# Performance work log

Measured on AMD Instinct MI355X. Metric: run time of the kernel, lower is better.

Reference implementation:

```python
import jax, jax.numpy as jnp
import numpy as np

N, C, H, W = 512, 64, 32, 32
HID, HEADS = 128, 4
E = 16384
BN_EPS = 1e-5


def conv2d(x, w, b, pad):
    y = jax.lax.conv_general_dilated(x, w, (1, 1), [(pad, pad), (pad, pad)],
                                     dimension_numbers=('NCHW', 'OIHW', 'NCHW'))
    return y + b[None, :, None, None]


def bn_eval(x, g, b):
    # inference BN with running_mean=0, running_var=1
    scale = g * (1.0 / np.sqrt(1.0 + BN_EPS))
    return x * scale[None, :, None, None] + b[None, :, None, None]


def gat_layer(x, src, dst, lin_w, att_s, att_d, bias):
    # x: (N, in) -> (N, HID); PyG GATConv heads=4, concat=False, add_self_loops
    h = (x @ lin_w).reshape(N, HEADS, HID)          # (N, H, D)
    a_s = jnp.einsum('nhd,hd->nh', h, att_s)        # source score
    a_d = jnp.einsum('nhd,hd->nh', h, att_d)        # target score
    e = jax.nn.leaky_relu(a_s[src] + a_d[dst], 0.2)  # (E', H)
    m = jax.ops.segment_max(e, dst, num_segments=N)
    ex = jnp.exp(e - m[dst])
    denom = jax.ops.segment_sum(ex, dst, num_segments=N)
    alpha = ex / (denom[dst] + 1e-16)               # per-target softmax
    out = jax.ops.segment_sum(alpha[:, :, None] * h[src], dst, num_segments=N)
    return out.mean(axis=1) + bias                  # concat=False -> head mean


def setup_inputs() -> dict:
    key = jax.random.key(0)
    ks = jax.random.split(key, 24)
    s = lambda *shape: 0.05
    d = {}
    d['x'] = jax.random.normal(ks[0], (N, C, H, W), jnp.float32)
    d['edge_index'] = jax.random.randint(ks[1], (2, E), 0, N, jnp.int64)
    d['confidence_maps'] = jax.random.uniform(ks[2], (N, 1, H, W), jnp.float32)
    # feature encoder: 1x1 conv + BN
    d['fe_w'] = jax.random.normal(ks[3], (HID, C, 1, 1), jnp.float32) * 0.05
    d['fe_b'] = jnp.zeros((HID,), jnp.float32)
    d['fe_g'] = jnp.ones((HID,), jnp.float32)
    d['fe_beta'] = jnp.zeros((HID,), jnp.float32)
    # spatial processor: two 3x3 conv + BN
    d['sp_w1'] = jax.random.normal(ks[4], (HID, HID, 3, 3), jnp.float32) * 0.02
    d['sp_b1'] = jnp.zeros((HID,), jnp.float32)
    d['sp_g1'] = jnp.ones((HID,), jnp.float32)
    d['sp_be1'] = jnp.zeros((HID,), jnp.float32)
    d['sp_w2'] = jax.random.normal(ks[5], (HID, HID, 3, 3), jnp.float32) * 0.02
    d['sp_b2'] = jnp.zeros((HID,), jnp.float32)
    d['sp_g2'] = jnp.ones((HID,), jnp.float32)
    d['sp_be2'] = jnp.zeros((HID,), jnp.float32)
    # GAT layers (in=HID, out=HID, heads=HEADS)
    d['g1_lin'] = jax.random.normal(ks[6], (HID, HEADS * HID), jnp.float32) * 0.05
    d['g1_as'] = jax.random.normal(ks[7], (HEADS, HID), jnp.float32) * 0.05
    d['g1_ad'] = jax.random.normal(ks[8], (HEADS, HID), jnp.float32) * 0.05
    d['g1_b'] = jnp.zeros((HID,), jnp.float32)
    d['g2_lin'] = jax.random.normal(ks[9], (HID, HEADS * HID), jnp.float32) * 0.05
    d['g2_as'] = jax.random.normal(ks[10], (HEADS, HID), jnp.float32) * 0.05
    d['g2_ad'] = jax.random.normal(ks[11], (HEADS, HID), jnp.float32) * 0.05
    d['g2_b'] = jnp.zeros((HID,), jnp.float32)
    # output projector 1x1 conv
    d['op_w'] = jax.random.normal(ks[12], (C, HID, 1, 1), jnp.float32) * 0.05
    d['op_b'] = jnp.zeros((C,), jnp.float32)
    return d


def reference(x, edge_index, confidence_maps, fe_w, fe_b, fe_g, fe_beta,
              sp_w1, sp_b1, sp_g1, sp_be1, sp_w2, sp_b2, sp_g2, sp_be2,
              g1_lin, g1_as, g1_ad, g1_b, g2_lin, g2_as, g2_ad, g2_b,
              op_w, op_b):
    # feature encoder + confidence modulation
    xe = jax.nn.relu(bn_eval(conv2d(x, fe_w, fe_b, 0), fe_g, fe_beta))
    xe = xe * confidence_maps
    # spatial processor
    xp = jax.nn.relu(bn_eval(conv2d(xe, sp_w1, sp_b1, 1), sp_g1, sp_be1))
    xp = jax.nn.relu(bn_eval(conv2d(xp, sp_w2, sp_b2, 1), sp_g2, sp_be2))
    # global avg pool -> node features (N, HID)
    x_node = xp.mean(axis=(2, 3))
    # add self loops once
    sl = jnp.arange(N, dtype=edge_index.dtype)
    src = jnp.concatenate([edge_index[0], sl])
    dst = jnp.concatenate([edge_index[1], sl])
    xg = jax.nn.relu(gat_layer(x_node, src, dst, g1_lin, g1_as, g1_ad, g1_b))
    xg = jax.nn.relu(gat_layer(xg, src, dst, g2_lin, g2_as, g2_ad, g2_b))
    # broadcast-add GNN output back onto spatial maps
    x_comb = xg[:, :, None, None] + xp
    return conv2d(x_comb, op_w, op_b, 0)
```

## Files before the change

### kernel.cpp

```cpp
#include <hip/hip_runtime.h>
#include <stdint.h>

#define NIMG 512
#define CINCH 64
#define HIDC 128
#define NEDGE 16384
#define HWPIX 1024
#define PW2 34
#define PPIX 1156
#define APITCH 272
#define AROW 9248

typedef __attribute__((ext_vector_type(8))) short bf16x8;
typedef __attribute__((ext_vector_type(4))) float f32x4;
typedef __attribute__((ext_vector_type(16))) float f32x16;

static __device__ __forceinline__ unsigned short f2bf(float f){
  unsigned u = __builtin_bit_cast(unsigned, f);
  u += 0x7FFFu + ((u>>16)&1u);
  return (unsigned short)(u>>16);
}
static __device__ __forceinline__ float bf2f(unsigned short s){
  unsigned u = ((unsigned)s)<<16;
  return __builtin_bit_cast(float, u);
}

static __device__ __forceinline__ void gload16(const char* src, char* dst){
  __builtin_amdgcn_global_load_lds(
      (const __attribute__((address_space(1))) unsigned int*)src,
      (__attribute__((address_space(3))) unsigned int*)dst, 16, 0, 0);
}

__global__ void k_init(unsigned short* xe_pad, unsigned short* xp1_pad,
                       float* xnode_acc, int* cnt, int* pos){
  int idx = blockIdx.x*256 + threadIdx.x;
  int total_b = NIMG*132*16;
  for(int i = idx; i < total_b; i += gridDim.x*256){
    int img = i / (132*16);
    int rem = i - img*(132*16);
    int bp = rem >> 4;
    int slot = rem & 15;
    int r, c;
    if(bp < 34){ r = 0; c = bp; }
    else if(bp < 68){ r = 33; c = bp-34; }
    else if(bp < 100){ r = bp-68+1; c = 0; }
    else { r = bp-100+1; c = 33; }
    size_t off = ((size_t)img*PPIX + r*PW2 + c)*128 + slot*8;
    uint4 z = {0,0,0,0};
    *(uint4*)(xe_pad + off) = z;
    *(uint4*)(xp1_pad + off) = z;
  }
  for(int i = idx; i < NIMG*HIDC; i += gridDim.x*256) xnode_acc[i] = 0.f;
  for(int i = idx; i < NIMG; i += gridDim.x*256){ cnt[i] = 0; pos[i] = 0; }
}

__global__ void k_wconv(const float* __restrict__ sp_w1, const float* __restrict__ sp_w2,
                        const float* __restrict__ fe_w, const float* __restrict__ op_w,
                        unsigned short* Wb1, unsigned short* Wb2,
                        unsigned short* Wfe, unsigned short* Wop){
  int idx = blockIdx.x*256 + threadIdx.x;
  for(int i = idx; i < 147456; i += gridDim.x*256){
    int j = i & 7, slot = (i>>3)&15, co = (i>>7)&127, tap = i>>14;
    int cin = (((slot - 3*co) & 15)<<3) + j;
    Wb1[i] = f2bf(sp_w1[(co*128+cin)*9 + tap]);
    Wb2[i] = f2bf(sp_w2[(co*128+cin)*9 + tap]);
  }
  for(int i = idx; i < 8192; i += gridDim.x*256){
    int j = i & 7, s = (i>>3)&7, co = i>>6;
    int ci = ((s ^ (co&7))<<3) + j;
    Wfe[i] = f2bf(fe_w[co*64+ci]);
  }
  for(int i = idx; i < 8192; i += gridDim.x*256){
    int j = i & 7, s = (i>>3)&15, co = i>>7;
    int cin = ((s ^ (co&7))<<3) + j;
    Wop[i] = f2bf(op_w[co*128+cin]);
  }
}

__global__ void k_csr_count(const int* __restrict__ ei, int* cnt){
  int e = blockIdx.x*256 + threadIdx.x;
  if(e < NEDGE) atomicAdd(&cnt[ei[NEDGE+e]], 1);
}
__global__ void k_csr_scan(const int* __restrict__ cnt, int* offs){
  __shared__ int sc[512];
  int t = threadIdx.x;
  sc[t] = cnt[t] + 1;
  __syncthreads();
  for(int o = 1; o < 512; o <<= 1){
    int add = (t >= o) ? sc[t-o] : 0;
    __syncthreads();
    sc[t] += add;
    __syncthreads();
  }
  if(t == 0) offs[0] = 0;
  offs[t+1] = sc[t];
}
__global__ void k_csr_fill(const int* __restrict__ ei, const int* __restrict__ offs,
                           int* pos, int* csr_src){
  int e = blockIdx.x*256 + threadIdx.x;
  if(e < NEDGE + NIMG){
    int s, d;
    if(e < NEDGE){ s = ei[e]; d = ei[NEDGE+e]; }
    else { s = e - NEDGE; d = s; }
    int slot = offs[d] + atomicAdd(&pos[d], 1);
    csr_src[slot] = s;
  }
}

__launch_bounds__(256, 2)
__global__ void k_encode(const float* __restrict__ x, const float* __restrict__ conf,
                         const unsigned short* __restrict__ Wfe,
                         const float* __restrict__ fe_b, const float* __restrict__ fe_g,
                         const float* __restrict__ fe_beta,
                         unsigned short* __restrict__ xe_pad){
  __shared__ char lds[49152];
  char* xa = lds; char* wb = lds + 32768;
  int tid = threadIdx.x;
  int n = blockIdx.x >> 3, rg = blockIdx.x & 7;
  int hw0 = rg*128;
  {
    int q = tid >> 3, c0 = tid & 7;
    const float* xb = x + (size_t)n*CINCH*HWPIX + hw0;
    #pragma unroll
    for(int cc = 0; cc < 8; ++cc){
      int c = cc*8 + c0;
      float4 v = *(const float4*)(xb + (size_t)c*HWPIX + q*4);
      float vv[4] = {v.x, v.y, v.z, v.w};
      #pragma unroll
      for(int i = 0; i < 4; ++i){
        int p = q*4 + i;
        *(float*)(xa + p*256 + ((cc ^ (p&7))*32) + c0*4) = vv[i];
      }
    }
    #pragma unroll
    for(int it = 0; it < 4; ++it){
      uint4 w = *(const uint4*)((const char*)Wfe + it*4096 + tid*16);
      *(uint4*)(wb + it*4096 + tid*16) = w;
    }
  }
  __syncthreads();
  int wid = tid>>6, lane = tid&63;
  int wr = wid>>1, wc = wid&1, fr = lane&15, fq = lane>>4;
  f32x4 acc[4][4];
  #pragma unroll
  for(int a = 0; a < 4; ++a)
    #pragma unroll
    for(int b = 0; b < 4; ++b) acc[a][b] = (f32x4){0.f,0.f,0.f,0.f};
  #pragma unroll
  for(int kc = 0; kc < 2; ++kc){
    bf16x8 af[4], bfr[4];
    #pragma unroll
    for(int mi = 0; mi < 4; ++mi){
      int p = wr*64 + mi*16 + fr;
      int u = kc*4 + fq;
      const float* src = (const float*)(xa + p*256 + ((u ^ (p&7))*32));
      float4 lo = *(const float4*)src;
      float4 hi = *(const float4*)(src+4);
      bf16x8 a;
      a[0]=(short)f2bf(lo.x); a[1]=(short)f2bf(lo.y); a[2]=(short)f2bf(lo.z); a[3]=(short)f2bf(lo.w);
      a[4]=(short)f2bf(hi.x); a[5]=(short)f2bf(hi.y); a[6]=(short)f2bf(hi.z); a[7]=(short)f2bf(hi.w);
      af[mi] = a;
    }
    #pragma unroll
    for(int nf = 0; nf < 4; ++nf){
      int co = wc*64 + nf*16 + fr;
      int slot = (kc*4 + fq) ^ (co&7);
      bfr[nf] = *(const bf16x8*)(wb + co*128 + slot*16);
    }
    #pragma unroll
    for(int mi = 0; mi < 4; ++mi)
      #pragma unroll
      for(int nf = 0; nf < 4; ++nf)
        acc[mi][nf] = __builtin_amdgcn_mfma_f32_16x16x32_bf16(af[mi], bfr[nf], acc[mi][nf], 0,0,0);
  }
  __syncthreads();
  {
    const float rs = 0.9999950000374997f;
    float kb[4], ks[4], kbe[4];
    #pragma unroll
    for(int nf = 0; nf < 4; ++nf){
      int co = wc*64 + nf*16 + fr;
      kb[nf] = fe_b[co]; ks[nf] = fe_g[co]*rs; kbe[nf] = fe_beta[co];
    }
    #pragma unroll
    for(int mi = 0; mi < 4; ++mi)
      #pragma unroll
      for(int j = 0; j < 4; ++j){
        int px = wr*64 + mi*16 + fq*4 + j;
        float cf = conf[(size_t)n*HWPIX + hw0 + px];
        #pragma unroll
        for(int nf = 0; nf < 4; ++nf){
          float v = (acc[mi][nf][j] + kb[nf])*ks[nf] + kbe[nf];
          v = fmaxf(v, 0.f)*cf;
          int co = wc*64 + nf*16 + fr;
          *(unsigned short*)(xa + px*256 + ((co*2) ^ (((px>>2)&7)<<4))) = f2bf(v);
        }
      }
  }
  __syncthreads();
  {
    int p = tid>>1, half = tid&1;
    int r = rg*4 + (p>>5), c = p&31;
    int key = 2*((p&31) + 1);
    unsigned short* dst = xe_pad + ((size_t)n*PPIX + (r+1)*PW2 + (c+1))*128;
    #pragma unroll
    for(int s = 0; s < 8; ++s){
      int ls = half*8 + s;
      uint4 v = *(uint4*)(xa + p*256 + ((ls*16) ^ (((p>>2)&7)<<4)));
      *(uint4*)(dst + ((ls + key)&15)*8) = v;
    }
  }
}

__launch_bounds__(256, 1)
__global__ void k_conv3(const unsigned short* __restrict__ inp,
                        const unsigned short* __restrict__ Wb,
                        const float* __restrict__ bnb, const float* __restrict__ bng,
                        const float* __restrict__ bnbe,
                        unsigned short* __restrict__ outp,
                        float* __restrict__ xnode_acc, int mode){
  extern __shared__ char lds[];
  char* Ab = lds;
  char* Wd = lds + 93184;
  int tid = threadIdx.x;
  int n = blockIdx.x>>2, rg = blockIdx.x&3;

  const char* img  = (const char*)inp + ((size_t)n*PPIX + (size_t)rg*8*PW2)*256;
  const char* wsrc = (const char*)Wb;

  #pragma unroll
  for(int it = 0; it < 8; ++it)
    gload16(wsrc + it*4096 + tid*16, Wd + it*4096 + tid*16);
  #pragma unroll
  for(int it = 0; it < 23; ++it){
    int j = tid + it*256;
    if(it < 22 || j < 5824){
      int pidx = j/17, s = j - pidx*17;
      if(pidx > 339) pidx = 339;
      if(s == 16) s = 0;
      gload16(img + (size_t)pidx*256 + s*16, Ab + (size_t)j*16);
    }
  }

  int wid = tid>>6, lane = tid&63;
  int wr = wid>>1, wc = wid&1;
  int col = lane&31, hi = lane>>5;
  int cob = (wc*64 + col)*256;

  f32x16 acc[4][2];
  #pragma unroll
  for(int a = 0; a < 4; ++a)
    #pragma unroll
    for(int b = 0; b < 2; ++b)
      #pragma unroll
      for(int r = 0; r < 16; ++r) acc[a][b][r] = 0.f;

  __syncthreads();

  for(int tap = 0; tap < 9; ++tap){
    if(tap < 8){
      const char* ws = wsrc + (size_t)(tap+1)*32768;
      char* wdst = Wd + ((tap+1)&1)*32768;
      #pragma unroll
      for(int it = 0; it < 8; ++it)
        gload16(ws + it*4096 + tid*16, wdst + it*4096 + tid*16);
    }
    const char* cur = Wd + (tap&1)*32768;
    int dy = tap/3 - 1, dx = tap - (tap/3)*3 - 1;
    int pcol = col + 1 + dx;
    int prow0 = wr*4 + 1 + dy;
    int a0 = prow0*AROW + pcol*APITCH;
    int ka = 2*pcol;
    #pragma unroll
    for(int kc = 0; kc < 8; ++kc){
      int g = kc*2 + hi;
      int sa = ((g + ka)&15)<<4;
      bf16x8 af0 = *(const bf16x8*)(Ab + a0 + sa);
      bf16x8 af1 = *(const bf16x8*)(Ab + a0 + AROW + sa);
      bf16x8 af2 = *(const bf16x8*)(Ab + a0 + 2*AROW + sa);
      bf16x8 af3 = *(const bf16x8*)(Ab + a0 + 3*AROW + sa);
      int sw = ((g + 3*col)&15)<<4;
      bf16x8 wf0 = *(const bf16x8*)(cur + cob + sw);
      bf16x8 wf1 = *(const bf16x8*)(cur + cob + 8192 + sw);
      acc[0][0] = __builtin_amdgcn_mfma_f32_32x32x16_bf16(af0, wf0, acc[0][0], 0,0,0);
      acc[0][1] = __builtin_amdgcn_mfma_f32_32x32x16_bf16(af0, wf1, acc[0][1], 0,0,0);
      acc[1][0] = __builtin_amdgcn_mfma_f32_32x32x16_bf16(af1, wf0, acc[1][0], 0,0,0);
      acc[1][1] = __builtin_amdgcn_mfma_f32_32x32x16_bf16(af1, wf1, acc[1][1], 0,0,0);
      acc[2][0] = __builtin_amdgcn_mfma_f32_32x32x16_bf16(af2, wf0, acc[2][0], 0,0,0);
      acc[2][1] = __builtin_amdgcn_mfma_f32_32x32x16_bf16(af2, wf1, acc[2][1], 0,0,0);
      acc[3][0] = __builtin_amdgcn_mfma_f32_32x32x16_bf16(af3, wf0, acc[3][0], 0,0,0);
      acc[3][1] = __builtin_amdgcn_mfma_f32_32x32x16_bf16(af3, wf1, acc[3][1], 0,0,0);
    }
    __syncthreads();
  }

  char* eb = Ab;
  float sn0 = 0.f, sn1 = 0.f;
  {
    const float rs = 0.9999950000374997f;
    float kb[2], ks[2], kbe[2];
    #pragma unroll
    for(int nf = 0; nf < 2; ++nf){
      int co = wc*64 + nf*32 + col;
      kb[nf] = bnb[co]; ks[nf] = bng[co]*rs; kbe[nf] = bnbe[co];
    }
    #pragma unroll
    for(int mi = 0; mi < 4; ++mi)
      #pragma unroll
      for(int reg = 0; reg < 16; ++reg){
        int pc = (reg&3) + 8*(reg>>2) + 4*hi;
        int px = (wr*4 + mi)*32 + pc;
        #pragma unroll
        for(int nf = 0; nf < 2; ++nf){
          float v = (acc[mi][nf][reg] + kb[nf])*ks[nf] + kbe[nf];
          v = fmaxf(v, 0.f);
          if(nf == 0) sn0 += v; else sn1 += v;
          int co = wc*64 + nf*32 + col;
          *(unsigned short*)(eb + px*256 + ((co*2) ^ (((px>>2)&7)<<4))) = f2bf(v);
        }
      }
  }
  if(mode == 1){
    sn0 += __shfl_down(sn0, 32);
    sn1 += __shfl_down(sn1, 32);
    if(lane < 32){
      atomicAdd(&xnode_acc[n*HIDC + wc*64 + col], sn0);
      atomicAdd(&xnode_acc[n*HIDC + wc*64 + 32 + col], sn1);
    }
  }
  __syncthreads();
  {
    int p = tid;
    int r = rg*8 + (p>>5), c = p&31;
    unsigned short* dst;
    int key;
    if(mode == 0){
      key = 2*((p&31) + 1);
      dst = outp + ((size_t)n*PPIX + (r+1)*PW2 + (c+1))*128;
    } else {
      key = 3*p;
      dst = outp + ((size_t)n*HWPIX + rg*256 + p)*128;
    }
    #pragma unroll
    for(int s = 0; s < 16; ++s){
      uint4 v = *(uint4*)(eb + p*256 + ((s*16) ^ (((p>>2)&7)<<4)));
      *(uint4*)(dst + ((s + key)&15)*8) = v;
    }
  }
}

__global__ void k_gat_lin(const float* __restrict__ xin, float scale,
                          const float* __restrict__ lin,
                          const float* __restrict__ as_, const float* __restrict__ ad_,
                          float* __restrict__ h, float* __restrict__ a_s, float* __restrict__ a_d){
  __shared__ float xs[128];
  __shared__ float rs0[4], rs1[4], rd0[4], rd1[4];
  int n = blockIdx.x, t = threadIdx.x;
  if(t < 128) xs[t] = xin[n*128 + t]*scale;
  __syncthreads();
  float o0 = 0.f, o1 = 0.f;
  for(int k = 0; k < 128; ++k){
    float xv = xs[k];
    o0 += xv*lin[k*512 + t];
    o1 += xv*lin[k*512 + t + 256];
  }
  h[(size_t)n*512 + t] = o0;
  h[(size_t)n*512 + t + 256] = o1;
  float s0 = o0*as_[t], s1 = o1*as_[t+256];
  float d0 = o0*ad_[t], d1 = o1*ad_[t+256];
  #pragma unroll
  for(int o = 32; o; o >>= 1){
    s0 += __shfl_down(s0, o); s1 += __shfl_down(s1, o);
    d0 += __shfl_down(d0, o); d1 += __shfl_down(d1, o);
  }
  int w = t>>6;
  if((t&63) == 0){ rs0[w]=s0; rs1[w]=s1; rd0[w]=d0; rd1[w]=d1; }
  __syncthreads();
  if(t < 4){
    if(t < 2){
      a_s[n*4+t] = rs0[2*t] + rs0[2*t+1];
      a_d[n*4+t] = rd0[2*t] + rd0[2*t+1];
    } else {
      a_s[n*4+t] = rs1[2*(t-2)] + rs1[2*(t-2)+1];
      a_d[n*4+t] = rd1[2*(t-2)] + rd1[2*(t-2)+1];
    }
  }
}

__global__ void k_gat_aggr(const int* __restrict__ offs, const int* __restrict__ csr_src,
                           const float* __restrict__ a_s, const float* __restrict__ a_d,
                           const float* __restrict__ h, const float* __restrict__ bias,
                           float* __restrict__ y){
  __shared__ int ssrc[2048];
  __shared__ float sex[4][2048];
  __shared__ float out4[512];
  __shared__ float adn[4], smax[4], sden[4];
  __shared__ float wred[4][4];
  int n = blockIdx.x, t = threadIdx.x;
  int base = offs[n], deg = offs[n+1] - base;
  if(t < 4) adn[t] = a_d[n*4 + t];
  __syncthreads();
  bool cached = (deg <= 2048);
  float lm0=-1e30f, lm1=-1e30f, lm2=-1e30f, lm3=-1e30f;
  for(int e = t; e < deg; e += 256){
    int s = csr_src[base + e];
    float v0 = a_s[s*4+0] + adn[0]; v0 = v0 > 0.f ? v0 : 0.2f*v0;
    float v1 = a_s[s*4+1] + adn[1]; v1 = v1 > 0.f ? v1 : 0.2f*v1;
    float v2 = a_s[s*4+2] + adn[2]; v2 = v2 > 0.f ? v2 : 0.2f*v2;
    float v3 = a_s[s*4+3] + adn[3]; v3 = v3 > 0.f ? v3 : 0.2f*v3;
    if(cached){ ssrc[e]=s; sex[0][e]=v0; sex[1][e]=v1; sex[2][e]=v2; sex[3][e]=v3; }
    lm0 = fmaxf(lm0, v0); lm1 = fmaxf(lm1, v1); lm2 = fmaxf(lm2, v2); lm3 = fmaxf(lm3, v3);
  }
  #pragma unroll
  for(int o = 32; o; o >>= 1){
    lm0 = fmaxf(lm0, __shfl_down(lm0, o)); lm1 = fmaxf(lm1, __shfl_down(lm1, o));
    lm2 = fmaxf(lm2, __shfl_down(lm2, o)); lm3 = fmaxf(lm3, __shfl_down(lm3, o));
  }
  int w = t>>6;
  if((t&63) == 0){ wred[w][0]=lm0; wred[w][1]=lm1; wred[w][2]=lm2; wred[w][3]=lm3; }
  __syncthreads();
  if(t < 4) smax[t] = fmaxf(fmaxf(wred[0][t], wred[1][t]), fmaxf(wred[2][t], wred[3][t]));
  __syncthreads();
  float m0 = smax[0], m1 = smax[1], m2 = smax[2], m3 = smax[3];
  float ls0=0.f, ls1=0.f, ls2=0.f, ls3=0.f;
  for(int e = t; e < deg; e += 256){
    float e0, e1, e2, e3;
    if(cached){ e0 = sex[0][e]; e1 = sex[1][e]; e2 = sex[2][e]; e3 = sex[3][e]; }
    else {
      int s = csr_src[base + e];
      e0 = a_s[s*4+0] + adn[0]; e0 = e0 > 0.f ? e0 : 0.2f*e0;
      e1 = a_s[s*4+1] + adn[1]; e1 = e1 > 0.f ? e1 : 0.2f*e1;
      e2 = a_s[s*4+2] + adn[2]; e2 = e2 > 0.f ? e2 : 0.2f*e2;
      e3 = a_s[s*4+3] + adn[3]; e3 = e3 > 0.f ? e3 : 0.2f*e3;
    }
    e0 = __expf(e0-m0); e1 = __expf(e1-m1); e2 = __expf(e2-m2); e3 = __expf(e3-m3);
    if(cached){ sex[0][e]=e0; sex[1][e]=e1; sex[2][e]=e2; sex[3][e]=e3; }
    ls0 += e0; ls1 += e1; ls2 += e2; ls3 += e3;
  }
  #pragma unroll
  for(int o = 32; o; o >>= 1){
    ls0 += __shfl_down(ls0, o); ls1 += __shfl_down(ls1, o);
    ls2 += __shfl_down(ls2, o); ls3 += __shfl_down(ls3, o);
  }
  __syncthreads();
  if((t&63) == 0){ wred[w][0]=ls0; wred[w][1]=ls1; wred[w][2]=ls2; wred[w][3]=ls3; }
  __syncthreads();
  if(t < 4) sden[t] = wred[0][t] + wred[1][t] + wred[2][t] + wred[3][t] + 1e-16f;
  __syncthreads();
  #pragma unroll
  for(int oo = 0; oo < 2; ++oo){
    int o = t + oo*256;
    int hd = o>>7, d = o&127;
    float mh = smax[hd];
    float accv = 0.f;
    for(int e = 0; e < deg; ++e){
      float ex; int s;
      if(cached){ ex = sex[hd][e]; s = ssrc[e]; }
      else {
        s = csr_src[base + e];
        float v = a_s[s*4+hd] + adn[hd]; v = v > 0.f ? v : 0.2f*v;
        ex = __expf(v - mh);
      }
      accv += ex * h[(size_t)s*512 + hd*128 + d];
    }
    out4[o] = accv / sden[hd];
  }
  __syncthreads();
  if(t < 128){
    float v = (out4[t] + out4[128+t] + out4[256+t] + out4[384+t])*0.25f + bias[t];
    y[n*128 + t] = fmaxf(v, 0.f);
  }
}

__global__ void k_nodebias(const float* __restrict__ xg2, const float* __restrict__ op_w,
                           const float* __restrict__ op_b, float* __restrict__ nb){
  int g = blockIdx.x*256 + threadIdx.x;
  if(g < NIMG*64){
    int n = g>>6, co = g&63;
    float acc = op_b[co];
    for(int k = 0; k < 128; ++k) acc += op_w[co*128+k]*xg2[n*128+k];
    nb[g] = acc;
  }
}

__launch_bounds__(256, 2)
__global__ void k_outconv(const unsigned short* __restrict__ xp2,
                          const unsigned short* __restrict__ Wop,
                          const float* __restrict__ nb, float* __restrict__ out){
  __shared__ char lds[16384];
  int tid = threadIdx.x;
  int n = blockIdx.x>>3, rg = blockIdx.x&7;
  #pragma unroll
  for(int it = 0; it < 4; ++it){
    uint4 v = *(const uint4*)((const char*)Wop + it*4096 + tid*16);
    *(uint4*)(lds + it*4096 + tid*16) = v;
  }
  __syncthreads();
  int wid = tid>>6, lane = tid&63;
  int wr = wid>>1, wc = wid&1, fr = lane&15, fq = lane>>4;
  f32x4 acc[4][2];
  #pragma unroll
  for(int a = 0; a < 4; ++a){ acc[a][0] = (f32x4){0.f,0.f,0.f,0.f}; acc[a][1] = (f32x4){0.f,0.f,0.f,0.f}; }
  const unsigned short* abase = xp2 + ((size_t)n*HWPIX + rg*128)*128;
  #pragma unroll
  for(int kc = 0; kc < 4; ++kc){
    bf16x8 af[4], bfr[2];
    #pragma unroll
    for(int mi = 0; mi < 4; ++mi){
      int p = wr*64 + mi*16 + fr;
      af[mi] = *(const bf16x8*)(abase + p*128 + (((kc*4+fq) + 3*p)&15)*8);
    }
    #pragma unroll
    for(int nf = 0; nf < 2; ++nf){
      int co = wc*32 + nf*16 + fr;
      int slot = (kc*4 + fq) ^ (co&7);
      bfr[nf] = *(const bf16x8*)(lds + co*256 + slot*16);
    }
    #pragma unroll
    for(int mi = 0; mi < 4; ++mi)
      #pragma unroll
      for(int nf = 0; nf < 2; ++nf)
        acc[mi][nf] = __builtin_amdgcn_mfma_f32_16x16x32_bf16(af[mi], bfr[nf], acc[mi][nf], 0,0,0);
  }
  #pragma unroll
  for(int mi = 0; mi < 4; ++mi)
    #pragma unroll
    for(int nf = 0; nf < 2; ++nf){
      int co = wc*32 + nf*16 + fr;
      int hw = rg*128 + wr*64 + mi*16 + fq*4;
      float nbv = nb[n*64 + co];
      float4 v = { acc[mi][nf][0]+nbv, acc[mi][nf][1]+nbv, acc[mi][nf][2]+nbv, acc[mi][nf][3]+nbv };
      *(float4*)(out + ((size_t)n*64 + co)*HWPIX + hw) = v;
    }
}

extern "C" void kernel_launch(void* const* d_in, const int* in_sizes, int n_in,
                              void* d_out, int out_size, void* d_ws, size_t ws_size,
                              hipStream_t stream){
  const float* x       = (const float*)d_in[0];
  const int*   ei      = (const int*)d_in[1];
  const float* conf    = (const float*)d_in[2];
  const float* fe_w    = (const float*)d_in[3];
  const float* fe_b    = (const float*)d_in[4];
  const float* fe_g    = (const float*)d_in[5];
  const float* fe_beta = (const float*)d_in[6];
  const float* sp_w1   = (const float*)d_in[7];
  const float* sp_b1   = (const float*)d_in[8];
  const float* sp_g1   = (const float*)d_in[9];
  const float* sp_be1  = (const float*)d_in[10];
  const float* sp_w2   = (const float*)d_in[11];
  const float* sp_b2   = (const float*)d_in[12];
  const float* sp_g2   = (const float*)d_in[13];
  const float* sp_be2  = (const float*)d_in[14];
  const float* g1_lin  = (const float*)d_in[15];
  const float* g1_as   = (const float*)d_in[16];
  const float* g1_ad   = (const float*)d_in[17];
  const float* g1_b    = (const float*)d_in[18];
  const float* g2_lin  = (const float*)d_in[19];
  const float* g2_as   = (const float*)d_in[20];
  const float* g2_ad   = (const float*)d_in[21];
  const float* g2_b    = (const float*)d_in[22];
  const float* op_w    = (const float*)d_in[23];
  const float* op_b    = (const float*)d_in[24];
  float* out = (float*)d_out;

  char* ws = (char*)d_ws;
  size_t off = 0;
  auto alloc = [&](size_t bytes)->char*{
    char* p = ws + off; off += (bytes + 255) & ~(size_t)255; return p;
  };
  unsigned short* bigA  = (unsigned short*)alloc((size_t)NIMG*PPIX*128*2);
  unsigned short* xp1   = (unsigned short*)alloc((size_t)NIMG*PPIX*128*2);
  unsigned short* Wb1   = (unsigned short*)alloc(147456*2);
  unsigned short* Wb2   = (unsigned short*)alloc(147456*2);
  unsigned short* Wfe   = (unsigned short*)alloc(8192*2);
  unsigned short* Wop   = (unsigned short*)alloc(8192*2);
  float* xnode_acc = (float*)alloc(NIMG*HIDC*4);
  float* h     = (float*)alloc((size_t)NIMG*512*4);
  float* a_s   = (float*)alloc(NIMG*4*4);
  float* a_d   = (float*)alloc(NIMG*4*4);
  float* xg1   = (float*)alloc(NIMG*HIDC*4);
  float* xg2   = (float*)alloc(NIMG*HIDC*4);
  int* cnt     = (int*)alloc(NIMG*4);
  int* pos     = (int*)alloc(NIMG*4);
  int* offs    = (int*)alloc((NIMG+1)*4);
  int* csr_src = (int*)alloc((NEDGE+NIMG)*4);
  float* nb    = (float*)alloc(NIMG*64*4);
  if(off > ws_size) return;
  unsigned short* xp2 = bigA;

  hipFuncSetAttribute((const void*)k_conv3,
                      hipFuncAttributeMaxDynamicSharedMemorySize, 158720);

  k_init<<<1024, 256, 0, stream>>>(bigA, xp1, xnode_acc, cnt, pos);
  k_wconv<<<576, 256, 0, stream>>>(sp_w1, sp_w2, fe_w, op_w, Wb1, Wb2, Wfe, Wop);
  k_csr_count<<<(NEDGE+255)/256, 256, 0, stream>>>(ei, cnt);
  k_csr_scan<<<1, 512, 0, stream>>>(cnt, offs);
  k_csr_fill<<<(NEDGE+NIMG+255)/256, 256, 0, stream>>>(ei, offs, pos, csr_src);
  k_encode<<<4096, 256, 0, stream>>>(x, conf, Wfe, fe_b, fe_g, fe_beta, bigA);
  k_conv3<<<2048, 256, 158720, stream>>>(bigA, Wb1, sp_b1, sp_g1, sp_be1, xp1, xnode_acc, 0);
  k_conv3<<<2048, 256, 158720, stream>>>(xp1, Wb2, sp_b2, sp_g2, sp_be2, xp2, xnode_acc, 1);
  k_gat_lin<<<512, 256, 0, stream>>>(xnode_acc, 1.f/1024.f, g1_lin, g1_as, g1_ad, h, a_s, a_d);
  k_gat_aggr<<<512, 256, 0, stream>>>(offs, csr_src, a_s, a_d, h, g1_b, xg1);
  k_gat_lin<<<512, 256, 0, stream>>>(xg1, 1.f, g2_lin, g2_as, g2_ad, h, a_s, a_d);
  k_gat_aggr<<<512, 256, 0, stream>>>(offs, csr_src, a_s, a_d, h, g2_b, xg2);
  k_nodebias<<<(NIMG*64+255)/256, 256, 0, stream>>>(xg2, op_w, op_b, nb);
  k_outconv<<<4096, 256, 0, stream>>>(xp2, Wop, nb, out);
}
```

Measured before the change: 624.6 us.

## Split conv3 input channels into two halves to halve LDS and fit two blocks

```diff
diff --git a/kernel.cpp b/kernel.cpp
--- a/kernel.cpp
+++ b/kernel.cpp
@@ -8,8 +8,8 @@
 #define HWPIX 1024
 #define PW2 34
 #define PPIX 1156
-#define APITCH 272
-#define AROW 9248
+#define APITCH 144
+#define AROW 4896
 
 typedef __attribute__((ext_vector_type(8))) short bf16x8;
 typedef __attribute__((ext_vector_type(4))) float f32x4;
@@ -60,8 +60,9 @@
                         unsigned short* Wfe, unsigned short* Wop){
   int idx = blockIdx.x*256 + threadIdx.x;
   for(int i = idx; i < 147456; i += gridDim.x*256){
-    int j = i & 7, slot = (i>>3)&15, co = (i>>7)&127, tap = i>>14;
-    int cin = (((slot - 3*co) & 15)<<3) + j;
+    int j = i & 7, pos = (i>>3)&7, co = (i>>6)&127, img = i>>13;
+    int h = img/9, tap = img - 9*h;
+    int cin = h*64 + (((pos - 3*co) & 7)<<3) + j;
     Wb1[i] = f2bf(sp_w1[(co*128+cin)*9 + tap]);
     Wb2[i] = f2bf(sp_w2[(co*128+cin)*9 + tap]);
   }
@@ -207,12 +208,13 @@
     for(int s = 0; s < 8; ++s){
       int ls = half*8 + s;
       uint4 v = *(uint4*)(xa + p*256 + ((ls*16) ^ (((p>>2)&7)<<4)));
-      *(uint4*)(dst + ((ls + key)&15)*8) = v;
-    }
-  }
-}
-
-__launch_bounds__(256, 1)
+      int pos = (ls>>3)*8 + (((ls&7) + key)&7);
+      *(uint4*)(dst + pos*8) = v;
+    }
+  }
+}
+
+__launch_bounds__(256, 2)
 __global__ void k_conv3(const unsigned short* __restrict__ inp,
                         const unsigned short* __restrict__ Wb,
                         const float* __restrict__ bnb, const float* __restrict__ bng,
@@ -221,7 +223,7 @@
                         float* __restrict__ xnode_acc, int mode){
   extern __shared__ char lds[];
   char* Ab = lds;
-  char* Wd = lds + 93184;
+  char* Wd = lds + 49152;
   int tid = threadIdx.x;
   int n = blockIdx.x>>2, rg = blockIdx.x&3;
 
@@ -229,23 +231,22 @@
   const char* wsrc = (const char*)Wb;
 
   #pragma unroll
-  for(int it = 0; it < 8; ++it)
+  for(int it = 0; it < 4; ++it)
     gload16(wsrc + it*4096 + tid*16, Wd + it*4096 + tid*16);
   #pragma unroll
-  for(int it = 0; it < 23; ++it){
+  for(int it = 0; it < 12; ++it){
     int j = tid + it*256;
-    if(it < 22 || j < 5824){
-      int pidx = j/17, s = j - pidx*17;
-      if(pidx > 339) pidx = 339;
-      if(s == 16) s = 0;
-      gload16(img + (size_t)pidx*256 + s*16, Ab + (size_t)j*16);
-    }
+    int q9 = j/9;
+    int s = j - 9*q9;
+    int pidx = q9 > 339 ? 339 : q9;
+    int ss = (s == 8) ? 0 : s;
+    gload16(img + (size_t)pidx*256 + 0*128 + ss*16, Ab + (size_t)j*16);
   }
 
   int wid = tid>>6, lane = tid&63;
   int wr = wid>>1, wc = wid&1;
   int col = lane&31, hi = lane>>5;
-  int cob = (wc*64 + col)*256;
+  int cob = (wc*64 + col)*128;
 
   f32x16 acc[4][2];
   #pragma unroll
@@ -257,44 +258,61 @@
 
   __syncthreads();
 
-  for(int tap = 0; tap < 9; ++tap){
-    if(tap < 8){
-      const char* ws = wsrc + (size_t)(tap+1)*32768;
-      char* wdst = Wd + ((tap+1)&1)*32768;
-      #pragma unroll
-      for(int it = 0; it < 8; ++it)
-        gload16(ws + it*4096 + tid*16, wdst + it*4096 + tid*16);
-    }
-    const char* cur = Wd + (tap&1)*32768;
-    int dy = tap/3 - 1, dx = tap - (tap/3)*3 - 1;
-    int pcol = col + 1 + dx;
-    int prow0 = wr*4 + 1 + dy;
-    int a0 = prow0*AROW + pcol*APITCH;
-    int ka = 2*pcol;
-    #pragma unroll
-    for(int kc = 0; kc < 8; ++kc){
-      int g = kc*2 + hi;
-      int sa = ((g + ka)&15)<<4;
-      bf16x8 af0 = *(const bf16x8*)(Ab + a0 + sa);
-      bf16x8 af1 = *(const bf16x8*)(Ab + a0 + AROW + sa);
-      bf16x8 af2 = *(const bf16x8*)(Ab + a0 + 2*AROW + sa);
-      bf16x8 af3 = *(const bf16x8*)(Ab + a0 + 3*AROW + sa);
-      int sw = ((g + 3*col)&15)<<4;
-      bf16x8 wf0 = *(const bf16x8*)(cur + cob + sw);
-      bf16x8 wf1 = *(const bf16x8*)(cur + cob + 8192 + sw);
-      acc[0][0] = __builtin_amdgcn_mfma_f32_32x32x16_bf16(af0, wf0, acc[0][0], 0,0,0);
-      acc[0][1] = __builtin_amdgcn_mfma_f32_32x32x16_bf16(af0, wf1, acc[0][1], 0,0,0);
-      acc[1][0] = __builtin_amdgcn_mfma_f32_32x32x16_bf16(af1, wf0, acc[1][0], 0,0,0);
-      acc[1][1] = __builtin_amdgcn_mfma_f32_32x32x16_bf16(af1, wf1, acc[1][1], 0,0,0);
-      acc[2][0] = __builtin_amdgcn_mfma_f32_32x32x16_bf16(af2, wf0, acc[2][0], 0,0,0);
-      acc[2][1] = __builtin_amdgcn_mfma_f32_32x32x16_bf16(af2, wf1, acc[2][1], 0,0,0);
-      acc[3][0] = __builtin_amdgcn_mfma_f32_32x32x16_bf16(af3, wf0, acc[3][0], 0,0,0);
-      acc[3][1] = __builtin_amdgcn_mfma_f32_32x32x16_bf16(af3, wf1, acc[3][1], 0,0,0);
-    }
-    __syncthreads();
-  }
-
-  char* eb = Ab;
+  for(int h = 0; h < 2; ++h){
+    if(h == 1){
+      #pragma unroll
+      for(int it = 0; it < 12; ++it){
+        int j = tid + it*256;
+        int q9 = j/9;
+        int s = j - 9*q9;
+        int pidx = q9 > 339 ? 339 : q9;
+        int ss = (s == 8) ? 0 : s;
+        gload16(img + (size_t)pidx*256 + 128 + ss*16, Ab + (size_t)j*16);
+      }
+      __syncthreads();
+    }
+    for(int tap = 0; tap < 9; ++tap){
+      int q = h*9 + tap;
+      if(q < 17){
+        const char* ws = wsrc + (size_t)(q+1)*16384;
+        char* wdst = Wd + ((q+1)&1)*16384;
+        #pragma unroll
+        for(int it = 0; it < 4; ++it)
+          gload16(ws + it*4096 + tid*16, wdst + it*4096 + tid*16);
+      }
+      const char* cur = Wd + (q&1)*16384;
+      int dy = tap/3 - 1, dx = tap - (tap/3)*3 - 1;
+      int pcol = col + 1 + dx;
+      int prow0 = wr*4 + 1 + dy;
+      int a0b = (prow0*34 + pcol)*APITCH;
+      int ka = 2*pcol;
+      __builtin_amdgcn_s_setprio(1);
+      #pragma unroll
+      for(int kc = 0; kc < 4; ++kc){
+        int g = kc*2 + hi;
+        int sa = ((g + ka)&7)<<4;
+        bf16x8 af0 = *(const bf16x8*)(Ab + a0b + sa);
+        bf16x8 af1 = *(const bf16x8*)(Ab + a0b + AROW + sa);
+        bf16x8 af2 = *(const bf16x8*)(Ab + a0b + 2*AROW + sa);
+        bf16x8 af3 = *(const bf16x8*)(Ab + a0b + 3*AROW + sa);
+        int sw = ((g + 3*col)&7)<<4;
+        bf16x8 wf0 = *(const bf16x8*)(cur + cob + sw);
+        bf16x8 wf1 = *(const bf16x8*)(cur + cob + 4096 + sw);
+        acc[0][0] = __builtin_amdgcn_mfma_f32_32x32x16_bf16(af0, wf0, acc[0][0], 0,0,0);
+        acc[0][1] = __builtin_amdgcn_mfma_f32_32x32x16_bf16(af0, wf1, acc[0][1], 0,0,0);
+        acc[1][0] = __builtin_amdgcn_mfma_f32_32x32x16_bf16(af1, wf0, acc[1][0], 0,0,0);
+        acc[1][1] = __builtin_amdgcn_mfma_f32_32x32x16_bf16(af1, wf1, acc[1][1], 0,0,0);
+        acc[2][0] = __builtin_amdgcn_mfma_f32_32x32x16_bf16(af2, wf0, acc[2][0], 0,0,0);
+        acc[2][1] = __builtin_amdgcn_mfma_f32_32x32x16_bf16(af2, wf1, acc[2][1], 0,0,0);
+        acc[3][0] = __builtin_amdgcn_mfma_f32_32x32x16_bf16(af3, wf0, acc[3][0], 0,0,0);
+        acc[3][1] = __builtin_amdgcn_mfma_f32_32x32x16_bf16(af3, wf1, acc[3][1], 0,0,0);
+      }
+      __builtin_amdgcn_s_setprio(0);
+      __syncthreads();
+    }
+  }
+
+  char* eb = lds;
   float sn0 = 0.f, sn1 = 0.f;
   {
     const float rs = 0.9999950000374997f;
@@ -344,7 +362,8 @@
     #pragma unroll
     for(int s = 0; s < 16; ++s){
       uint4 v = *(uint4*)(eb + p*256 + ((s*16) ^ (((p>>2)&7)<<4)));
-      *(uint4*)(dst + ((s + key)&15)*8) = v;
+      int pos = (s>>3)*8 + (((s&7) + key)&7);
+      *(uint4*)(dst + pos*8) = v;
     }
   }
 }
@@ -508,7 +527,9 @@
     #pragma unroll
     for(int mi = 0; mi < 4; ++mi){
       int p = wr*64 + mi*16 + fr;
-      af[mi] = *(const bf16x8*)(abase + p*128 + (((kc*4+fq) + 3*p)&15)*8);
+      int G = kc*4 + fq;
+      int pos = (G>>3)*8 + (((G&7) + 3*p)&7);
+      af[mi] = *(const bf16x8*)(abase + p*128 + pos*8);
     }
     #pragma unroll
     for(int nf = 0; nf < 2; ++nf){
@@ -590,7 +611,7 @@
   unsigned short* xp2 = bigA;
 
   hipFuncSetAttribute((const void*)k_conv3,
-                      hipFuncAttributeMaxDynamicSharedMemorySize, 158720);
+                      hipFuncAttributeMaxDynamicSharedMemorySize, 81920);
 
   k_init<<<1024, 256, 0, stream>>>(bigA, xp1, xnode_acc, cnt, pos);
   k_wconv<<<576, 256, 0, stream>>>(sp_w1, sp_w2, fe_w, op_w, Wb1, Wb2, Wfe, Wop);
@@ -598,8 +619,8 @@
   k_csr_scan<<<1, 512, 0, stream>>>(cnt, offs);
   k_csr_fill<<<(NEDGE+NIMG+255)/256, 256, 0, stream>>>(ei, offs, pos, csr_src);
   k_encode<<<4096, 256, 0, stream>>>(x, conf, Wfe, fe_b, fe_g, fe_beta, bigA);
-  k_conv3<<<2048, 256, 158720, stream>>>(bigA, Wb1, sp_b1, sp_g1, sp_be1, xp1, xnode_acc, 0);
-  k_conv3<<<2048, 256, 158720, stream>>>(xp1, Wb2, sp_b2, sp_g2, sp_be2, xp2, xnode_acc, 1);
+  k_conv3<<<2048, 256, 81920, stream>>>(bigA, Wb1, sp_b1, sp_g1, sp_be1, xp1, xnode_acc, 0);
+  k_conv3<<<2048, 256, 81920, stream>>>(xp1, Wb2, sp_b2, sp_g2, sp_be2, xp2, xnode_acc, 1);
   k_gat_lin<<<512, 256, 0, stream>>>(xnode_acc, 1.f/1024.f, g1_lin, g1_as, g1_ad, h, a_s, a_d);
   k_gat_aggr<<<512, 256, 0, stream>>>(offs, csr_src, a_s, a_d, h, g1_b, xg1);
   k_gat_lin<<<512, 256, 0, stream>>>(xg1, 1.f, g2_lin, g2_as, g2_ad, h, a_s, a_d);
```

Measured after the change: 554.4 us. 11.2% less time.
